# Kernel optimization log

Hardware: AMD Instinct MI355X
Metric: run time of the kernel (lower is better)

## Reference

```python
import jax, jax.numpy as jnp
import numpy as np

DILATIONS = [1, 2, 4, 8, 16, 32, 64, 128, 256, 512]
C = 256   # channels
K = 3     # kernel size


def causal_conv(x, w, b, d):
    # x: [B, C_in, T], w: [C_out, C_in, K] -> [B, C_out, T], left-padded causal
    y = jax.lax.conv_general_dilated(
        x, w,
        window_strides=(1,),
        padding=[((K - 1) * d, 0)],
        rhs_dilation=(d,),
        dimension_numbers=('NCH', 'OIH', 'NCH'))
    return y + b[None, :, None]


def setup_inputs() -> dict:
    key = jax.random.key(0)
    ks = jax.random.split(key, 5)
    L = len(DILATIONS)
    B, T = 4, 8192
    s = 0.05  # weight scale
    return {
        'input': jax.random.normal(ks[0], (B, C, T), jnp.float32),
        'weights_conv': jax.random.normal(ks[1], (L, 2 * C, C, K), jnp.float32) * s,
        'biases_conv': jax.random.normal(ks[2], (L, 2 * C), jnp.float32) * s,
        'weights_out': jax.random.normal(ks[3], (L, C, C), jnp.float32) * s,
        'biases_out': jax.random.normal(ks[4], (L, C), jnp.float32) * s,
    }


def reference(input, weights_conv, biases_conv, weights_out, biases_out):
    x = input  # [B, C, T]
    L = len(DILATIONS)
    skips = []
    for i, d in enumerate(DILATIONS):
        z = causal_conv(x, weights_conv[i], biases_conv[i], d)  # [B, 2C, T]
        # gated activation: tanh on first half, sigmoid on second half
        h = jnp.tanh(z[:, :C]) * jax.nn.sigmoid(z[:, C:])       # [B, C, T]
        skips.append(h)
        if i < L - 1:
            # 1x1 output transform (disabled on the last layer)
            out = jnp.einsum('oc,bct->bot', weights_out[i], h) + biases_out[i][None, :, None]
        else:
            out = h
        x = out + x  # residual connection applied in the stack
    return x, jnp.stack(skips, axis=0)  # ([B,C,T], [L,B,C,T])
```

## Files before the change

kernel.cpp:

```cpp
#include <hip/hip_runtime.h>
#include <hip/hip_bf16.h>

#define BATCH 4
#define CCH 256
#define TLEN 8192
#define LAYERS 10
#define BCT (BATCH*CCH*TLEN)
#define TPAD 1024
#define TROWS (TPAD + TLEN)

typedef __attribute__((ext_vector_type(8))) short bf16x8;
typedef __attribute__((ext_vector_type(4))) float f32x4;

__device__ __forceinline__ unsigned short f2b(float f) {
  union { float f; unsigned u; } v; v.f = f;
  unsigned r = (v.u + 0x7FFFu + ((v.u >> 16) & 1u)) >> 16;
  return (unsigned short)r;
}
__device__ __forceinline__ float b2f(unsigned short h) {
  union { unsigned u; float f; } v; v.u = ((unsigned)h) << 16;
  return v.f;
}

__device__ __forceinline__ void gload16(const void* g, void* l) {
  __builtin_amdgcn_global_load_lds((__attribute__((address_space(1))) void*)g,
                                   (__attribute__((address_space(3))) void*)l, 16, 0, 0);
}

__device__ __forceinline__ float fast_tanh(float x) {
  float a = fabsf(x);
  float e = __expf(-2.f * a);
  float th = (1.f - e) * __builtin_amdgcn_rcpf(1.f + e);
  return copysignf(th, x);
}
__device__ __forceinline__ float fast_sigmoid(float x) {
  return __builtin_amdgcn_rcpf(1.f + __expf(-x));
}

__global__ void repack_w(const float* __restrict__ wc, const float* __restrict__ wo,
                         unsigned short* __restrict__ Wb, unsigned short* __restrict__ Wob) {
  size_t g = (size_t)blockIdx.x * 256 + threadIdx.x;
  const size_t NA = (size_t)LAYERS * 3 * 2 * 256 * 256;
  if (g < NA) {
    int c   = (int)(g & 255);
    int row = (int)((g >> 8) & 255);
    int y   = (int)((g >> 16) & 1);
    int lt  = (int)(g >> 17);
    int tap = lt % 3, l = lt / 3;
    int ch = y * 128 + ((row >> 5) << 4) + (row & 15) + (((row >> 4) & 1) << 8);
    Wb[g] = f2b(wc[(((size_t)l * 512 + ch) * 256 + c) * 3 + tap]);
  } else {
    size_t g2 = g - NA;
    if (g2 < (size_t)LAYERS * 256 * 256) Wob[g2] = f2b(wo[g2]);
  }
}

__global__ void zero_pads(unsigned short* __restrict__ xTb) {
  size_t off = (size_t)blockIdx.y * TROWS * CCH;
  int i = blockIdx.x * 256 + threadIdx.x;
  ulonglong2 z; z.x = 0ull; z.y = 0ull;
  ((ulonglong2*)(xTb + off))[i] = z;
}

__global__ void transpose_in(const float* __restrict__ in, float* __restrict__ xT,
                             unsigned short* __restrict__ xTb) {
  __shared__ float tile[32][33];
  const int tid = threadIdx.x;
  const int t0 = blockIdx.x * 32, c0 = blockIdx.y * 32, b = blockIdx.z;
#pragma unroll
  for (int q = 0; q < 4; ++q) {
    int e = tid + 256 * q; int r = e >> 5, cc = e & 31;
    tile[r][cc] = in[((size_t)b * CCH + c0 + r) * TLEN + t0 + cc];
  }
  __syncthreads();
#pragma unroll
  for (int q = 0; q < 4; ++q) {
    int e = tid + 256 * q; int r = e >> 5, cc = e & 31;
    float v = tile[cc][r];
    xT[((size_t)b * TLEN + t0 + r) * CCH + c0 + cc] = v;
    xTb[((size_t)b * TROWS + TPAD + t0 + r) * CCH + c0 + cc] = f2b(v);
  }
}

__global__ void final_addT(const float* __restrict__ xT, const unsigned short* __restrict__ hT,
                           float* __restrict__ out) {
  __shared__ float tile[32][33];
  const int tid = threadIdx.x;
  const int t0 = blockIdx.x * 32, c0 = blockIdx.y * 32, b = blockIdx.z;
#pragma unroll
  for (int q = 0; q < 4; ++q) {
    int e = tid + 256 * q; int r = e >> 5, cc = e & 31;
    size_t idx = ((size_t)b * TLEN + t0 + r) * CCH + c0 + cc;
    tile[r][cc] = xT[idx] + b2f(hT[idx]);
  }
  __syncthreads();
#pragma unroll
  for (int q = 0; q < 4; ++q) {
    int e = tid + 256 * q; int r = e >> 5, cc = e & 31;
    out[((size_t)b * CCH + c0 + r) * TLEN + t0 + cc] = tile[cc][r];
  }
}

__global__ __launch_bounds__(512, 2)
void conv_gate_kernel(const unsigned short* __restrict__ xTb,
                      const unsigned short* __restrict__ Wl,
                      const float* __restrict__ bias,
                      unsigned short* __restrict__ hT,
                      float* __restrict__ skip,
                      int d) {
  __shared__ __align__(16) unsigned short As[3][256 * 32];
  __shared__ __align__(16) unsigned short Bs[3][256 * 32];

  const int tid  = threadIdx.x;
  const int lane = tid & 63;
  const int wv   = tid >> 6;
  const int wm   = wv & 1;
  const int wn   = wv >> 1;
  const int col  = lane & 15, quad = lane >> 4;

  const int bid  = blockIdx.x;
  const int swzb = (bid & 7) * 32 + (bid >> 3);
  const int t0   = (swzb & 31) * 256;
  const int y    = (swzb >> 5) & 1;
  const int b    = swzb >> 6;

  const int srow  = lane >> 2;
  const int sslot = lane & 3;

  const unsigned short* Arow = xTb + ((size_t)b * TROWS + TPAD + t0) * CCH;

  f32x4 acc[8][4];
  const f32x4 zero = {0.f, 0.f, 0.f, 0.f};
#pragma unroll
  for (int i = 0; i < 8; ++i)
#pragma unroll
    for (int j = 0; j < 4; ++j) acc[i][j] = zero;

  const int NT = 24;

  auto stageA = [&](int kt, int slot) {
    const int tap = kt >> 3, c0 = (kt & 7) << 5;
    const unsigned short* Ab = Arow - (size_t)((2 - tap) * d) * CCH + c0;
#pragma unroll
    for (int j = 0; j < 2; ++j) {
      const int row = (wv * 2 + j) * 16 + srow;
      const int ss  = sslot ^ ((row >> 1) & 3);
      gload16(Ab + (size_t)row * CCH + ss * 8, &As[slot][(wv * 2 + j) * 512]);
    }
  };
  auto stageB = [&](int kt, int slot) {
    const int tap = kt >> 3, c0 = (kt & 7) << 5;
    const unsigned short* Wp = Wl + ((size_t)(tap * 2 + y)) * (256 * 256) + c0;
#pragma unroll
    for (int j = 0; j < 2; ++j) {
      const int row = (wv * 2 + j) * 16 + srow;
      const int ss  = sslot ^ ((row >> 1) & 3);
      gload16(Wp + (size_t)row * 256 + ss * 8, &Bs[slot][(wv * 2 + j) * 512]);
    }
  };

  auto ktile = [&](int slot, int stageKt, bool vm4) {
    if (vm4) asm volatile("s_waitcnt vmcnt(4)" ::: "memory");
    else     asm volatile("s_waitcnt vmcnt(0)" ::: "memory");
    __builtin_amdgcn_s_barrier();
    const int pslot = (slot + 2) % 3;
    bf16x8 bf[4], af[4];
#pragma unroll
    for (int nf = 0; nf < 4; ++nf) {
      const int row = wn * 64 + nf * 16 + col;
      bf[nf] = *(const bf16x8*)&Bs[slot][row * 32 + ((quad ^ ((row >> 1) & 3)) << 3)];
    }
#pragma unroll
    for (int mf = 0; mf < 4; ++mf) {
      const int row = wm * 128 + mf * 16 + col;
      af[mf] = *(const bf16x8*)&As[slot][row * 32 + ((quad ^ ((row >> 1) & 3)) << 3)];
    }
    if (stageKt >= 0) stageA(stageKt, pslot);
    __builtin_amdgcn_s_setprio(1);
#pragma unroll
    for (int mf = 0; mf < 4; ++mf)
#pragma unroll
      for (int nf = 0; nf < 4; ++nf)
        acc[mf][nf] = __builtin_amdgcn_mfma_f32_16x16x32_bf16(af[mf], bf[nf], acc[mf][nf], 0, 0, 0);
    __builtin_amdgcn_s_setprio(0);
    __builtin_amdgcn_sched_barrier(0);
#pragma unroll
    for (int mf = 0; mf < 4; ++mf) {
      const int row = wm * 128 + (mf + 4) * 16 + col;
      af[mf] = *(const bf16x8*)&As[slot][row * 32 + ((quad ^ ((row >> 1) & 3)) << 3)];
    }
    if (stageKt >= 0) stageB(stageKt, pslot);
    __builtin_amdgcn_s_setprio(1);
#pragma unroll
    for (int mf = 0; mf < 4; ++mf)
#pragma unroll
      for (int nf = 0; nf < 4; ++nf)
        acc[mf + 4][nf] = __builtin_amdgcn_mfma_f32_16x16x32_bf16(af[mf], bf[nf], acc[mf + 4][nf], 0, 0, 0);
    __builtin_amdgcn_s_setprio(0);
    asm volatile("s_waitcnt lgkmcnt(0)" ::: "memory");
    __builtin_amdgcn_sched_barrier(0);
  };

  stageA(0, 0); stageB(0, 0);
  stageA(1, 1); stageB(1, 1);

#pragma unroll 1
  for (int kt = 0; kt < 21; kt += 3) {
    ktile(0, kt + 2, true);
    ktile(1, kt + 3, true);
    ktile(2, kt + 4, true);
  }
  ktile(0, 23, true);
  ktile(1, -1, true);
  ktile(2, -1, false);

#pragma unroll
  for (int p = 0; p < 2; ++p) {
    const int chn = y * 128 + (wn * 2 + p) * 16 + col;
    const float btop = bias[chn];
    const float bbot = bias[chn + 256];
    const size_t skipBase = ((size_t)b * CCH + chn) * TLEN;
#pragma unroll
    for (int mf = 0; mf < 8; ++mf) {
      const int tb = t0 + wm * 128 + mf * 16 + quad * 4;
      f32x4 zt = acc[mf][2 * p];
      f32x4 zb = acc[mf][2 * p + 1];
      float hr[4];
#pragma unroll
      for (int r = 0; r < 4; ++r) {
        float h = fast_tanh(zt[r] + btop) * fast_sigmoid(zb[r] + bbot);
        hr[r] = h;
        hT[((size_t)b * TLEN + tb + r) * CCH + chn] = f2b(h);
      }
      float4 hv; hv.x = hr[0]; hv.y = hr[1]; hv.z = hr[2]; hv.w = hr[3];
      *(float4*)&skip[skipBase + tb] = hv;
    }
  }
}

__global__ __launch_bounds__(256)
void onexone_kernel(const unsigned short* __restrict__ hT,
                    const unsigned short* __restrict__ Wo,
                    const float* __restrict__ bias,
                    float* __restrict__ xT,
                    unsigned short* __restrict__ xTb) {
  __shared__ unsigned short As[2][128 * 32];
  __shared__ unsigned short Bs[2][128 * 32];

  const int tid  = threadIdx.x;
  const int lane = tid & 63;
  const int wv   = tid >> 6;
  const int wm   = wv & 1, wn = wv >> 1;
  const int col  = lane & 15, quad = lane >> 4;

  const int t0 = blockIdx.x * 128;
  const int o0 = blockIdx.y * 128;
  const int b  = blockIdx.z;

  const int rl = lane >> 2;
  const int kl = (lane & 3) * 8;
  const int ch0 = wv * 2;

  const unsigned short* Ab = hT + (size_t)b * TLEN * CCH + (size_t)t0 * CCH;
  const unsigned short* Wb = Wo + (size_t)o0 * 256;

  f32x4 acc[4][4];
  const f32x4 zero = {0.f, 0.f, 0.f, 0.f};
#pragma unroll
  for (int i = 0; i < 4; ++i)
#pragma unroll
    for (int j = 0; j < 4; ++j) acc[i][j] = zero;

  const int NCHUNK = 8;

  auto stage = [&](int idx, int buf) {
    const int c0 = idx << 5;
    gload16(Ab + (size_t)(ch0 * 16      + rl) * CCH + c0 + kl, &As[buf][ ch0      * 512]);
    gload16(Ab + (size_t)(ch0 * 16 + 16 + rl) * CCH + c0 + kl, &As[buf][(ch0 + 1) * 512]);
    gload16(Wb + (size_t)(ch0 * 16      + rl) * 256 + c0 + kl, &Bs[buf][ ch0      * 512]);
    gload16(Wb + (size_t)(ch0 * 16 + 16 + rl) * 256 + c0 + kl, &Bs[buf][(ch0 + 1) * 512]);
  };

  auto step = [&](int buf, int next_idx) {
    const int k0 = quad * 8;
    bf16x8 af[4], bfv[4];
#pragma unroll
    for (int mf = 0; mf < 4; ++mf)
      af[mf] = *(const bf16x8*)&As[buf][(wm * 64 + mf * 16 + col) * 32 + k0];
#pragma unroll
    for (int nf = 0; nf < 4; ++nf)
      bfv[nf] = *(const bf16x8*)&Bs[buf][(wn * 64 + nf * 16 + col) * 32 + k0];
    if (next_idx < NCHUNK) stage(next_idx, buf ^ 1);
#pragma unroll
    for (int mf = 0; mf < 4; ++mf)
#pragma unroll
      for (int nf = 0; nf < 4; ++nf)
        acc[mf][nf] = __builtin_amdgcn_mfma_f32_16x16x32_bf16(af[mf], bfv[nf], acc[mf][nf], 0, 0, 0);
  };

  stage(0, 0);
  __syncthreads();
#pragma unroll 1
  for (int i = 0; i < NCHUNK; i += 2) {
    step(0, i + 1); __syncthreads();
    step(1, i + 2); __syncthreads();
  }

#pragma unroll
  for (int mf = 0; mf < 4; ++mf) {
    const int tb = t0 + wm * 64 + mf * 16 + quad * 4;
#pragma unroll
    for (int nf = 0; nf < 4; ++nf) {
      const int ch = o0 + wn * 64 + nf * 16 + col;
      const float bo = bias[ch];
#pragma unroll
      for (int r = 0; r < 4; ++r) {
        size_t idx = ((size_t)b * TLEN + tb + r) * CCH + ch;
        float nv = xT[idx] + acc[mf][nf][r] + bo;
        xT[idx] = nv;
        xTb[((size_t)b * TROWS + TPAD + tb + r) * CCH + ch] = f2b(nv);
      }
    }
  }
}

extern "C" void kernel_launch(void* const* d_in, const int* in_sizes, int n_in,
                              void* d_out, int out_size, void* d_ws, size_t ws_size,
                              hipStream_t stream) {
  const float* input = (const float*)d_in[0];
  const float* wconv = (const float*)d_in[1];
  const float* bconv = (const float*)d_in[2];
  const float* wout  = (const float*)d_in[3];
  const float* bout  = (const float*)d_in[4];
  float* out   = (float*)d_out;
  float* skips = out + (size_t)BCT;

  char* ws = (char*)d_ws;
  float*          xT  = (float*)ws;
  unsigned short* xTb = (unsigned short*)(ws + (size_t)BCT * 4);
  unsigned short* hT  = (unsigned short*)(ws + (size_t)BCT * 4
                                             + (size_t)BATCH * TROWS * CCH * 2);
  unsigned short* Wb  = hT + (size_t)BCT;
  unsigned short* Wob = Wb + (size_t)LAYERS * 3 * 512 * 256;

  static const int dil[LAYERS] = {1, 2, 4, 8, 16, 32, 64, 128, 256, 512};

  repack_w<<<17920, 256, 0, stream>>>(wconv, wout, Wb, Wob);
  zero_pads<<<dim3(128, BATCH), 256, 0, stream>>>(xTb);
  transpose_in<<<dim3(TLEN / 32, CCH / 32, BATCH), 256, 0, stream>>>(input, xT, xTb);

  for (int l = 0; l < LAYERS; ++l) {
    conv_gate_kernel<<<256, 512, 0, stream>>>(
        xTb, Wb + (size_t)l * 3 * 512 * 256, bconv + (size_t)l * 512,
        hT, skips + (size_t)l * BCT, dil[l]);
    if (l < LAYERS - 1) {
      onexone_kernel<<<dim3(TLEN / 128, 2, BATCH), 256, 0, stream>>>(
          hT, Wob + (size_t)l * 256 * 256, bout + (size_t)l * 256, xT, xTb);
    } else {
      final_addT<<<dim3(TLEN / 32, CCH / 32, BATCH), 256, 0, stream>>>(xT, hT, out);
    }
  }
}
```

Measured before the change: 981.9 us.

## Triple-buffer 1x1 GEMM with swizzled LDS and vectorize transpose kernels

The onexone kernel moves from double buffering with full __syncthreads to a three-slot LDS pipeline. It uses explicit vmcnt waits, XOR-swizzled LDS layout to avoid bank conflicts, and setprio around the MFMAs, copying the scheme already used in conv_gate_kernel. The transpose_in and final_addT kernels switch to 64x64 tiles with float4 and u16x4 vector loads and stores. Tuning vmcnt and barriers by hand risks subtle ordering bugs, and the larger LDS footprint may reduce occupancy.

```diff
diff --git a/kernel.cpp b/kernel.cpp
--- a/kernel.cpp
+++ b/kernel.cpp
@@ -11,6 +11,7 @@
 
 typedef __attribute__((ext_vector_type(8))) short bf16x8;
 typedef __attribute__((ext_vector_type(4))) float f32x4;
+typedef __attribute__((ext_vector_type(4))) unsigned short u16x4;
 
 __device__ __forceinline__ unsigned short f2b(float f) {
   union { float f; unsigned u; } v; v.f = f;
@@ -62,42 +63,59 @@
   ((ulonglong2*)(xTb + off))[i] = z;
 }
 
-__global__ void transpose_in(const float* __restrict__ in, float* __restrict__ xT,
-                             unsigned short* __restrict__ xTb) {
-  __shared__ float tile[32][33];
+__global__ __launch_bounds__(256)
+void transpose_in(const float* __restrict__ in, float* __restrict__ xT,
+                  unsigned short* __restrict__ xTb) {
+  __shared__ float tile[64][65];
   const int tid = threadIdx.x;
-  const int t0 = blockIdx.x * 32, c0 = blockIdx.y * 32, b = blockIdx.z;
-#pragma unroll
-  for (int q = 0; q < 4; ++q) {
-    int e = tid + 256 * q; int r = e >> 5, cc = e & 31;
-    tile[r][cc] = in[((size_t)b * CCH + c0 + r) * TLEN + t0 + cc];
+  const int t0 = blockIdx.x * 64, c0 = blockIdx.y * 64, b = blockIdx.z;
+  const int q4 = (tid & 15) * 4, r0 = tid >> 4;
+#pragma unroll
+  for (int p = 0; p < 4; ++p) {
+    const int r = r0 + 16 * p;
+    float4 v = *(const float4*)&in[((size_t)b * CCH + c0 + r) * TLEN + t0 + q4];
+    tile[r][q4 + 0] = v.x; tile[r][q4 + 1] = v.y;
+    tile[r][q4 + 2] = v.z; tile[r][q4 + 3] = v.w;
   }
   __syncthreads();
 #pragma unroll
-  for (int q = 0; q < 4; ++q) {
-    int e = tid + 256 * q; int r = e >> 5, cc = e & 31;
-    float v = tile[cc][r];
-    xT[((size_t)b * TLEN + t0 + r) * CCH + c0 + cc] = v;
-    xTb[((size_t)b * TROWS + TPAD + t0 + r) * CCH + c0 + cc] = f2b(v);
-  }
-}
-
-__global__ void final_addT(const float* __restrict__ xT, const unsigned short* __restrict__ hT,
-                           float* __restrict__ out) {
-  __shared__ float tile[32][33];
+  for (int p = 0; p < 4; ++p) {
+    const int tr = r0 + 16 * p;
+    float4 v;
+    v.x = tile[q4 + 0][tr]; v.y = tile[q4 + 1][tr];
+    v.z = tile[q4 + 2][tr]; v.w = tile[q4 + 3][tr];
+    *(float4*)&xT[((size_t)b * TLEN + t0 + tr) * CCH + c0 + q4] = v;
+    u16x4 h; h.x = f2b(v.x); h.y = f2b(v.y); h.z = f2b(v.z); h.w = f2b(v.w);
+    *(u16x4*)&xTb[((size_t)b * TROWS + TPAD + t0 + tr) * CCH + c0 + q4] = h;
+  }
+}
+
+__global__ __launch_bounds__(256)
+void final_addT(const float* __restrict__ xT, const unsigned short* __restrict__ hT,
+                float* __restrict__ out) {
+  __shared__ float tile[64][65];
   const int tid = threadIdx.x;
-  const int t0 = blockIdx.x * 32, c0 = blockIdx.y * 32, b = blockIdx.z;
-#pragma unroll
-  for (int q = 0; q < 4; ++q) {
-    int e = tid + 256 * q; int r = e >> 5, cc = e & 31;
-    size_t idx = ((size_t)b * TLEN + t0 + r) * CCH + c0 + cc;
-    tile[r][cc] = xT[idx] + b2f(hT[idx]);
+  const int t0 = blockIdx.x * 64, c0 = blockIdx.y * 64, b = blockIdx.z;
+  const int q4 = (tid & 15) * 4, r0 = tid >> 4;
+#pragma unroll
+  for (int p = 0; p < 4; ++p) {
+    const int tr = r0 + 16 * p;
+    size_t idx = ((size_t)b * TLEN + t0 + tr) * CCH + c0 + q4;
+    float4 x = *(const float4*)&xT[idx];
+    u16x4 h = *(const u16x4*)&hT[idx];
+    tile[tr][q4 + 0] = x.x + b2f(h.x);
+    tile[tr][q4 + 1] = x.y + b2f(h.y);
+    tile[tr][q4 + 2] = x.z + b2f(h.z);
+    tile[tr][q4 + 3] = x.w + b2f(h.w);
   }
   __syncthreads();
 #pragma unroll
-  for (int q = 0; q < 4; ++q) {
-    int e = tid + 256 * q; int r = e >> 5, cc = e & 31;
-    out[((size_t)b * CCH + c0 + r) * TLEN + t0 + cc] = tile[cc][r];
+  for (int p = 0; p < 4; ++p) {
+    const int c = r0 + 16 * p;
+    float4 v;
+    v.x = tile[q4 + 0][c]; v.y = tile[q4 + 1][c];
+    v.z = tile[q4 + 2][c]; v.w = tile[q4 + 3][c];
+    *(float4*)&out[((size_t)b * CCH + c0 + c) * TLEN + t0 + q4] = v;
   }
 }
 
@@ -136,8 +154,6 @@
 #pragma unroll
     for (int j = 0; j < 4; ++j) acc[i][j] = zero;
 
-  const int NT = 24;
-
   auto stageA = [&](int kt, int slot) {
     const int tap = kt >> 3, c0 = (kt & 7) << 5;
     const unsigned short* Ab = Arow - (size_t)((2 - tap) * d) * CCH + c0;
@@ -238,14 +254,14 @@
   }
 }
 
-__global__ __launch_bounds__(256)
+__global__ __launch_bounds__(256, 2)
 void onexone_kernel(const unsigned short* __restrict__ hT,
                     const unsigned short* __restrict__ Wo,
                     const float* __restrict__ bias,
                     float* __restrict__ xT,
                     unsigned short* __restrict__ xTb) {
-  __shared__ unsigned short As[2][128 * 32];
-  __shared__ unsigned short Bs[2][128 * 32];
+  __shared__ __align__(16) unsigned short As[3][128 * 32];
+  __shared__ __align__(16) unsigned short Bs[3][128 * 32];
 
   const int tid  = threadIdx.x;
   const int lane = tid & 63;
@@ -257,11 +273,10 @@
   const int o0 = blockIdx.y * 128;
   const int b  = blockIdx.z;
 
-  const int rl = lane >> 2;
-  const int kl = (lane & 3) * 8;
-  const int ch0 = wv * 2;
-
-  const unsigned short* Ab = hT + (size_t)b * TLEN * CCH + (size_t)t0 * CCH;
+  const int srow  = lane >> 2;
+  const int sslot = lane & 3;
+
+  const unsigned short* Ab = hT + ((size_t)b * TLEN + t0) * CCH;
   const unsigned short* Wb = Wo + (size_t)o0 * 256;
 
   f32x4 acc[4][4];
@@ -271,40 +286,58 @@
 #pragma unroll
     for (int j = 0; j < 4; ++j) acc[i][j] = zero;
 
-  const int NCHUNK = 8;
-
-  auto stage = [&](int idx, int buf) {
-    const int c0 = idx << 5;
-    gload16(Ab + (size_t)(ch0 * 16      + rl) * CCH + c0 + kl, &As[buf][ ch0      * 512]);
-    gload16(Ab + (size_t)(ch0 * 16 + 16 + rl) * CCH + c0 + kl, &As[buf][(ch0 + 1) * 512]);
-    gload16(Wb + (size_t)(ch0 * 16      + rl) * 256 + c0 + kl, &Bs[buf][ ch0      * 512]);
-    gload16(Wb + (size_t)(ch0 * 16 + 16 + rl) * 256 + c0 + kl, &Bs[buf][(ch0 + 1) * 512]);
-  };
-
-  auto step = [&](int buf, int next_idx) {
-    const int k0 = quad * 8;
-    bf16x8 af[4], bfv[4];
+  auto stage = [&](int kt, int slot) {
+    const int c0 = kt << 5;
+#pragma unroll
+    for (int j = 0; j < 2; ++j) {
+      const int row = (wv * 2 + j) * 16 + srow;
+      const int ss  = sslot ^ ((row >> 1) & 3);
+      gload16(Ab + (size_t)row * CCH + c0 + ss * 8, &As[slot][(wv * 2 + j) * 512]);
+    }
+#pragma unroll
+    for (int j = 0; j < 2; ++j) {
+      const int row = (wv * 2 + j) * 16 + srow;
+      const int ss  = sslot ^ ((row >> 1) & 3);
+      gload16(Wb + (size_t)row * 256 + c0 + ss * 8, &Bs[slot][(wv * 2 + j) * 512]);
+    }
+  };
+
+  auto ktile = [&](int slot, int stageKt, bool vm4) {
+    if (vm4) asm volatile("s_waitcnt vmcnt(4)" ::: "memory");
+    else     asm volatile("s_waitcnt vmcnt(0)" ::: "memory");
+    __builtin_amdgcn_s_barrier();
+    bf16x8 af[4], bf[4];
+#pragma unroll
+    for (int nf = 0; nf < 4; ++nf) {
+      const int row = wn * 64 + nf * 16 + col;
+      bf[nf] = *(const bf16x8*)&Bs[slot][row * 32 + ((quad ^ ((row >> 1) & 3)) << 3)];
+    }
+#pragma unroll
+    for (int mf = 0; mf < 4; ++mf) {
+      const int row = wm * 64 + mf * 16 + col;
+      af[mf] = *(const bf16x8*)&As[slot][row * 32 + ((quad ^ ((row >> 1) & 3)) << 3)];
+    }
+    if (stageKt >= 0) stage(stageKt, (slot + 2) % 3);
+    __builtin_amdgcn_s_setprio(1);
 #pragma unroll
     for (int mf = 0; mf < 4; ++mf)
-      af[mf] = *(const bf16x8*)&As[buf][(wm * 64 + mf * 16 + col) * 32 + k0];
-#pragma unroll
-    for (int nf = 0; nf < 4; ++nf)
-      bfv[nf] = *(const bf16x8*)&Bs[buf][(wn * 64 + nf * 16 + col) * 32 + k0];
-    if (next_idx < NCHUNK) stage(next_idx, buf ^ 1);
-#pragma unroll
-    for (int mf = 0; mf < 4; ++mf)
 #pragma unroll
       for (int nf = 0; nf < 4; ++nf)
-        acc[mf][nf] = __builtin_amdgcn_mfma_f32_16x16x32_bf16(af[mf], bfv[nf], acc[mf][nf], 0, 0, 0);
-  };
-
-  stage(0, 0);
-  __syncthreads();
-#pragma unroll 1
-  for (int i = 0; i < NCHUNK; i += 2) {
-    step(0, i + 1); __syncthreads();
-    step(1, i + 2); __syncthreads();
-  }
+        acc[mf][nf] = __builtin_amdgcn_mfma_f32_16x16x32_bf16(af[mf], bf[nf], acc[mf][nf], 0, 0, 0);
+    __builtin_amdgcn_s_setprio(0);
+    asm volatile("s_waitcnt lgkmcnt(0)" ::: "memory");
+    __builtin_amdgcn_sched_barrier(0);
+  };
+
+  stage(0, 0); stage(1, 1);
+  ktile(0, 2, true);
+  ktile(1, 3, true);
+  ktile(2, 4, true);
+  ktile(0, 5, true);
+  ktile(1, 6, true);
+  ktile(2, 7, true);
+  ktile(0, -1, true);
+  ktile(1, -1, false);
 
 #pragma unroll
   for (int mf = 0; mf < 4; ++mf) {
@@ -347,7 +380,7 @@
 
   repack_w<<<17920, 256, 0, stream>>>(wconv, wout, Wb, Wob);
   zero_pads<<<dim3(128, BATCH), 256, 0, stream>>>(xTb);
-  transpose_in<<<dim3(TLEN / 32, CCH / 32, BATCH), 256, 0, stream>>>(input, xT, xTb);
+  transpose_in<<<dim3(TLEN / 64, CCH / 64, BATCH), 256, 0, stream>>>(input, xT, xTb);
 
   for (int l = 0; l < LAYERS; ++l) {
     conv_gate_kernel<<<256, 512, 0, stream>>>(
@@ -357,7 +390,7 @@
       onexone_kernel<<<dim3(TLEN / 128, 2, BATCH), 256, 0, stream>>>(
           hT, Wob + (size_t)l * 256 * 256, bout + (size_t)l * 256, xT, xTb);
     } else {
-      final_addT<<<dim3(TLEN / 32, CCH / 32, BATCH), 256, 0, stream>>>(xT, hT, out);
-    }
-  }
-}
+      final_addT<<<dim3(TLEN / 64, CCH / 64, BATCH), 256, 0, stream>>>(xT, hT, out);
+    }
+  }
+}
```

Measured after the change: 985.0 us. Within noise of the previous version (+0.3%).
